# Kernel optimization log

Hardware: AMD Instinct MI355X
Metric: run time of the kernel (lower is better)

The kernel has to match this reference:

```python
import jax, jax.numpy as jnp
import numpy as np

N_EMBD = 2048
N_HEAD = 32
N_KV_HEAD = 8
HEAD_DIM = N_EMBD // N_HEAD  # 64
N_REP = N_HEAD // N_KV_HEAD  # 4
B, T = 2, 2048


def setup_inputs() -> dict:
    key = jax.random.key(0)
    ks = jax.random.split(key, 9)
    s = 1.0 / np.sqrt(N_EMBD)
    kv_dim = N_KV_HEAD * HEAD_DIM
    return {
        "x": jax.random.normal(ks[0], (B, T, N_EMBD), dtype=jnp.float32),
        "Wq": jax.random.normal(ks[1], (N_EMBD, N_EMBD), dtype=jnp.float32) * s,
        "bq": jax.random.normal(ks[2], (N_EMBD,), dtype=jnp.float32) * 0.01,
        "Wk": jax.random.normal(ks[3], (N_EMBD, kv_dim), dtype=jnp.float32) * s,
        "bk": jax.random.normal(ks[4], (kv_dim,), dtype=jnp.float32) * 0.01,
        "Wv": jax.random.normal(ks[5], (N_EMBD, kv_dim), dtype=jnp.float32) * s,
        "bv": jax.random.normal(ks[6], (kv_dim,), dtype=jnp.float32) * 0.01,
        "Wo": jax.random.normal(ks[7], (N_EMBD, N_EMBD), dtype=jnp.float32) * s,
        "bo": jax.random.normal(ks[8], (N_EMBD,), dtype=jnp.float32) * 0.01,
    }


def reference(x, Wq, bq, Wk, bk, Wv, bv, Wo, bo):
    Bsz, Tlen, C = x.shape
    # projections
    q = (x @ Wq + bq).reshape(Bsz, Tlen, N_HEAD, HEAD_DIM).transpose(0, 2, 1, 3)   # [B,H,T,d]
    k = (x @ Wk + bk).reshape(Bsz, Tlen, N_KV_HEAD, HEAD_DIM).transpose(0, 2, 1, 3)  # [B,Hkv,T,d]
    v = (x @ Wv + bv).reshape(Bsz, Tlen, N_KV_HEAD, HEAD_DIM).transpose(0, 2, 1, 3)
    # repeat_interleave KV heads to match query heads
    k = jnp.repeat(k, N_REP, axis=1)  # [B,H,T,d]
    v = jnp.repeat(v, N_REP, axis=1)
    # causal SDPA
    scale = 1.0 / jnp.sqrt(jnp.asarray(HEAD_DIM, dtype=x.dtype))
    scores = jnp.einsum('bhqd,bhkd->bhqk', q, k) * scale  # [B,H,T,T]
    causal = jnp.tril(jnp.ones((Tlen, Tlen), dtype=bool))
    scores = jnp.where(causal, scores, jnp.asarray(-jnp.inf, dtype=scores.dtype))
    attn = jax.nn.softmax(scores, axis=-1)
    y = jnp.einsum('bhqk,bhkd->bhqd', attn, v)  # [B,H,T,d]
    y = y.transpose(0, 2, 1, 3).reshape(Bsz, Tlen, C)
    return y @ Wo + bo
```

## Files before the change

kernel.cpp:

```cpp
#include <hip/hip_runtime.h>
#include <hip/hip_bf16.h>

#define B_SZ   2
#define T_SEQ  2048
#define C_EMB  2048
#define KV_DIM 512

typedef __bf16 bf16x8 __attribute__((ext_vector_type(8)));
typedef __bf16 bf16x4 __attribute__((ext_vector_type(4)));
typedef float  f32x4  __attribute__((ext_vector_type(4)));
typedef float  f32x16 __attribute__((ext_vector_type(16)));
typedef unsigned int u32;

typedef __attribute__((address_space(1))) const unsigned int gu32;
typedef __attribute__((address_space(3))) unsigned int lu32;
__device__ __forceinline__ void gload16(const void* g, void* l) {
  __builtin_amdgcn_global_load_lds((gu32*)g, (lu32*)l, 16, 0, 0);
}

__global__ __launch_bounds__(256) void cast_f32_bf16(const float* __restrict__ in,
                                                     __bf16* __restrict__ out, int n8) {
  int i = blockIdx.x * 256 + threadIdx.x;
  if (i < n8) {
    const float4* p = (const float4*)(in + (size_t)i * 8);
    float4 a = p[0], b = p[1];
    bf16x8 o;
    o[0] = (__bf16)a.x; o[1] = (__bf16)a.y; o[2] = (__bf16)a.z; o[3] = (__bf16)a.w;
    o[4] = (__bf16)b.x; o[5] = (__bf16)b.y; o[6] = (__bf16)b.z; o[7] = (__bf16)b.w;
    *(bf16x8*)(out + (size_t)i * 8) = o;
  }
}

__global__ __launch_bounds__(256) void transpose_cast_kernel(const float* __restrict__ in,
                                                             __bf16* __restrict__ out,
                                                             int R, int C) {
  __shared__ float tile[64][65];
  int c0 = blockIdx.x * 64, r0 = blockIdx.y * 64;
  int tid = threadIdx.x;
#pragma unroll
  for (int i = 0; i < 4; i++) {
    int idx = tid + i * 256;
    int row = idx >> 4;
    int c4  = (idx & 15) * 4;
    float4 v = *(const float4*)&in[(size_t)(r0 + row) * C + c0 + c4];
    tile[row][c4 + 0] = v.x; tile[row][c4 + 1] = v.y;
    tile[row][c4 + 2] = v.z; tile[row][c4 + 3] = v.w;
  }
  __syncthreads();
#pragma unroll
  for (int i = 0; i < 4; i++) {
    int idx = tid + i * 256;
    int col = idx >> 4;
    int r4  = (idx & 15) * 4;
    bf16x4 o;
    o[0] = (__bf16)tile[r4 + 0][col];
    o[1] = (__bf16)tile[r4 + 1][col];
    o[2] = (__bf16)tile[r4 + 2][col];
    o[3] = (__bf16)tile[r4 + 3][col];
    *(bf16x4*)&out[(size_t)(c0 + col) * R + r0 + r4] = o;
  }
}

__global__ __launch_bounds__(256) void concat_bias(const float* __restrict__ bq,
                                                   const float* __restrict__ bk,
                                                   const float* __restrict__ bv,
                                                   float* __restrict__ bcat) {
  int i = blockIdx.x * 256 + threadIdx.x;
  if (i < 3072) {
    float v = (i < 2048) ? bq[i] : (i < 2560 ? bk[i - 2048] : bv[i - 2560]);
    bcat[i] = v;
  }
}

template <int MODE>
__global__ __launch_bounds__(256) void gemm_bt(const __bf16* __restrict__ A,
                                               const __bf16* __restrict__ Bt,
                                               const float* __restrict__ bias,
                                               void* __restrict__ out0,
                                               __bf16* __restrict__ outK,
                                               __bf16* __restrict__ outV,
                                               int M, int N, int K) {
  __shared__ __bf16 As[128 * 32];
  __shared__ __bf16 Bs[128 * 32];
  int tid  = threadIdx.x;
  int lane = tid & 63, wave = tid >> 6;
  int wr = wave >> 1, wc = wave & 1;
  int la = lane & 15, kg = lane >> 4;
  int m0 = blockIdx.x * 128, n0 = blockIdx.y * 128;

  f32x4 acc[4][4];
#pragma unroll
  for (int i = 0; i < 4; i++)
#pragma unroll
    for (int j = 0; j < 4; j++)
#pragma unroll
      for (int r = 0; r < 4; r++) acc[i][j][r] = 0.f;

  int s0 = tid, s1 = tid + 256;
  const __bf16* ga0 = A  + (size_t)(m0 + (s0 >> 2)) * K + (s0 & 3) * 8;
  const __bf16* ga1 = A  + (size_t)(m0 + (s1 >> 2)) * K + (s1 & 3) * 8;
  const __bf16* gb0 = Bt + (size_t)(n0 + (s0 >> 2)) * K + (s0 & 3) * 8;
  const __bf16* gb1 = Bt + (size_t)(n0 + (s1 >> 2)) * K + (s1 & 3) * 8;
  __bf16* lA0 = As + (size_t)(0 * 256 + wave * 64) * 8;
  __bf16* lA1 = As + (size_t)(1 * 256 + wave * 64) * 8;
  __bf16* lB0 = Bs + (size_t)(0 * 256 + wave * 64) * 8;
  __bf16* lB1 = Bs + (size_t)(1 * 256 + wave * 64) * 8;

  for (int k0 = 0; k0 < K; k0 += 32) {
    gload16(ga0 + k0, lA0);
    gload16(ga1 + k0, lA1);
    gload16(gb0 + k0, lB0);
    gload16(gb1 + k0, lB1);
    __syncthreads();
    bf16x8 af[4], bfr[4];
#pragma unroll
    for (int i = 0; i < 4; i++) af[i]  = *(const bf16x8*)&As[(size_t)(wr * 64 + i * 16 + la) * 32 + kg * 8];
#pragma unroll
    for (int j = 0; j < 4; j++) bfr[j] = *(const bf16x8*)&Bs[(size_t)(wc * 64 + j * 16 + la) * 32 + kg * 8];
#pragma unroll
    for (int i = 0; i < 4; i++)
#pragma unroll
      for (int j = 0; j < 4; j++)
        acc[i][j] = __builtin_amdgcn_mfma_f32_16x16x32_bf16(af[i], bfr[j], acc[i][j], 0, 0, 0);
    __syncthreads();
  }

  int kgsw = ((kg & 1) << 1) | (kg >> 1);
#pragma unroll
  for (int i = 0; i < 4; i++) {
    int rowb  = m0 + wr * 64 + i * 16 + kg * 4;
    int rowbV = m0 + wr * 64 + i * 16 + kgsw * 4;
#pragma unroll
    for (int j = 0; j < 4; j++) {
      int col = n0 + wc * 64 + j * 16 + la;
      float bv = bias[col];
#pragma unroll
      for (int r = 0; r < 4; r++) {
        float v = acc[i][j][r] + bv;
        if (MODE == 2) {
          ((float*)out0)[(size_t)(rowb + r) * N + col] = v;
        } else {
          if (n0 < 2048)      ((__bf16*)out0)[(size_t)(rowb + r) * 2048 + col] = (__bf16)(v * 0.18033688f);
          else if (n0 < 2560) outK[(size_t)(rowb + r) * 512 + (col - 2048)] = (__bf16)v;
          else                outV[(size_t)(col - 2560) * M + rowbV + r] = (__bf16)v;
        }
      }
    }
  }
}

__global__ __launch_bounds__(128) void attn_kernel(const __bf16* __restrict__ Q,
                                                   const __bf16* __restrict__ K,
                                                   const __bf16* __restrict__ Vt,
                                                   __bf16* __restrict__ Y) {
  __shared__ __bf16 Ylds[2][32][72];
  const int M = B_SZ * T_SEQ;
  int tid = threadIdx.x;
  int wv = tid >> 6, l = tid & 63;
  int qcol = l & 31, hh = l >> 5;
  int g = blockIdx.x;
  int swz = (g & 7) * 128 + (g >> 3);
  int bh = swz >> 4, pi2 = swz & 15;
  int pi = pi2 * 2 + wv;
  int b = bh >> 5, hq = bh & 31, kvh = hq >> 2;

  const __bf16* kbase = K + (size_t)(b * T_SEQ + qcol) * KV_DIM + kvh * 64 + hh * 8;
  const __bf16* vb0 = Vt + (size_t)(kvh * 64 + qcol) * M + (size_t)b * T_SEQ + hh * 8;
  const __bf16* vb1 = vb0 + (size_t)32 * M;
  __bf16 (*slab)[72] = Ylds[wv];

  for (int halfi = 0; halfi < 2; ++halfi) {
    int qt = halfi ? (63 - pi) : pi;
    int q0 = qt * 32;

    const __bf16* qrow = Q + (size_t)(b * T_SEQ + q0 + qcol) * C_EMB + hq * 64;
    bf16x8 qf[4];
#pragma unroll
    for (int c = 0; c < 4; c++) qf[c] = *(const bf16x8*)(qrow + c * 16 + hh * 8);

    f32x16 acc0, acc1;
#pragma unroll
    for (int r = 0; r < 16; r++) { acc0[r] = 0.f; acc1[r] = 0.f; }
    float m_run = -1e30f, l_run = 0.f;

    bf16x8 kf[4];
#pragma unroll
    for (int c = 0; c < 4; c++) kf[c] = *(const bf16x8*)(kbase + c * 16);

    for (int kb = 0; kb <= q0; kb += 32) {
      f32x16 s;
#pragma unroll
      for (int r = 0; r < 16; r++) s[r] = 0.f;
      __builtin_amdgcn_s_setprio(1);
#pragma unroll
      for (int c = 0; c < 4; c++)
        s = __builtin_amdgcn_mfma_f32_32x32x16_bf16(kf[c], qf[c], s, 0, 0, 0);
      __builtin_amdgcn_s_setprio(0);
      {
        int nkb = (kb + 32 <= q0) ? kb + 32 : 0;
        const __bf16* nk = kbase + (size_t)nkb * KV_DIM;
#pragma unroll
        for (int c = 0; c < 4; c++) kf[c] = *(const bf16x8*)(nk + c * 16);
      }
      bf16x8 vf0 = *(const bf16x8*)(vb0 + kb);
      bf16x8 vf1 = *(const bf16x8*)(vb0 + kb + 16);
      bf16x8 vf2 = *(const bf16x8*)(vb1 + kb);
      bf16x8 vf3 = *(const bf16x8*)(vb1 + kb + 16);
      if (kb == q0) {
#pragma unroll
        for (int r = 0; r < 16; r++) {
          int kr = (r & 3) + 8 * (r >> 2) + 4 * hh;
          s[r] = (kr <= qcol) ? s[r] : -1e30f;
        }
      }
      float m01 = fmaxf(s[0], s[1]),  m23 = fmaxf(s[2], s[3]);
      float m45 = fmaxf(s[4], s[5]),  m67 = fmaxf(s[6], s[7]);
      float m89 = fmaxf(s[8], s[9]),  mab = fmaxf(s[10], s[11]);
      float mcd = fmaxf(s[12], s[13]), mef = fmaxf(s[14], s[15]);
      float mloc = fmaxf(fmaxf(fmaxf(m01, m23), fmaxf(m45, m67)),
                         fmaxf(fmaxf(m89, mab), fmaxf(mcd, mef)));
      mloc = fmaxf(mloc, __shfl_xor(mloc, 32, 64));
      if (__any(mloc > m_run + 6.0f)) {
        float mnew = fmaxf(m_run, mloc);
        float corr = exp2f(m_run - mnew);
        l_run *= corr;
#pragma unroll
        for (int r = 0; r < 16; r++) { acc0[r] *= corr; acc1[r] *= corr; }
        m_run = mnew;
      }
#pragma unroll
      for (int r = 0; r < 16; r++) s[r] = exp2f(s[r] - m_run);
      l_run += (((s[0] + s[1]) + (s[2] + s[3])) + ((s[4] + s[5]) + (s[6] + s[7])))
             + (((s[8] + s[9]) + (s[10] + s[11])) + ((s[12] + s[13]) + (s[14] + s[15])));
      union { u32 u[4]; bf16x8 v; } w0u, w1u;
#pragma unroll
      for (int j = 0; j < 4; j++) {
        union { __bf16 b2[2]; u32 u; } p0, p1;
        p0.b2[0] = (__bf16)s[2 * j];     p0.b2[1] = (__bf16)s[2 * j + 1];
        p1.b2[0] = (__bf16)s[8 + 2 * j]; p1.b2[1] = (__bf16)s[9 + 2 * j];
        w0u.u[j] = p0.u;
        w1u.u[j] = p1.u;
      }
      __builtin_amdgcn_s_setprio(1);
      acc0 = __builtin_amdgcn_mfma_f32_32x32x16_bf16(vf0, w0u.v, acc0, 0, 0, 0);
      acc0 = __builtin_amdgcn_mfma_f32_32x32x16_bf16(vf1, w1u.v, acc0, 0, 0, 0);
      acc1 = __builtin_amdgcn_mfma_f32_32x32x16_bf16(vf2, w0u.v, acc1, 0, 0, 0);
      acc1 = __builtin_amdgcn_mfma_f32_32x32x16_bf16(vf3, w1u.v, acc1, 0, 0, 0);
      __builtin_amdgcn_s_setprio(0);
    }

    l_run += __shfl_xor(l_run, 32, 64);
    float inv = 1.0f / l_run;
#pragma unroll
    for (int r = 0; r < 16; r++) {
      int drow = (r & 3) + 8 * (r >> 2) + 4 * hh;
      slab[qcol][drow]      = (__bf16)(acc0[r] * inv);
      slab[qcol][32 + drow] = (__bf16)(acc1[r] * inv);
    }
    __bf16* yrow = Y + (size_t)(b * T_SEQ + q0 + qcol) * C_EMB + hq * 64 + hh * 32;
#pragma unroll
    for (int c = 0; c < 4; c++)
      *(bf16x8*)(yrow + c * 8) = *(const bf16x8*)&slab[qcol][hh * 32 + c * 8];
  }
}

extern "C" void kernel_launch(void* const* d_in, const int* in_sizes, int n_in,
                              void* d_out, int out_size, void* d_ws, size_t ws_size,
                              hipStream_t stream) {
  const float* x  = (const float*)d_in[0];
  const float* Wq = (const float*)d_in[1];
  const float* bq = (const float*)d_in[2];
  const float* Wk = (const float*)d_in[3];
  const float* bk = (const float*)d_in[4];
  const float* Wv = (const float*)d_in[5];
  const float* bv = (const float*)d_in[6];
  const float* Wo = (const float*)d_in[7];
  const float* bo = (const float*)d_in[8];
  float* out = (float*)d_out;

  const int M = B_SZ * T_SEQ;

  char* w = (char*)d_ws;
  __bf16* xb   = (__bf16*)w; w += (size_t)M * C_EMB * 2;
  __bf16* Wall = (__bf16*)w; w += (size_t)3072 * C_EMB * 2;
  __bf16* Wot  = (__bf16*)w; w += (size_t)C_EMB * C_EMB * 2;
  float*  bcat = (float*)w;  w += (size_t)3072 * 4;
  __bf16* qb   = (__bf16*)w; w += (size_t)M * C_EMB * 2;
  __bf16* kbf  = (__bf16*)w; w += (size_t)M * KV_DIM * 2;
  __bf16* vbt  = (__bf16*)w; w += (size_t)KV_DIM * M * 2;
  __bf16* yb   = (__bf16*)w; w += (size_t)M * C_EMB * 2;

  cast_f32_bf16<<<(M * C_EMB / 8 + 255) / 256, 256, 0, stream>>>(x, xb, M * C_EMB / 8);

  transpose_cast_kernel<<<dim3(C_EMB / 64, C_EMB / 64), 256, 0, stream>>>(Wq, Wall, C_EMB, C_EMB);
  transpose_cast_kernel<<<dim3(KV_DIM / 64, C_EMB / 64), 256, 0, stream>>>(Wk, Wall + (size_t)2048 * C_EMB, C_EMB, KV_DIM);
  transpose_cast_kernel<<<dim3(KV_DIM / 64, C_EMB / 64), 256, 0, stream>>>(Wv, Wall + (size_t)2560 * C_EMB, C_EMB, KV_DIM);
  transpose_cast_kernel<<<dim3(C_EMB / 64, C_EMB / 64), 256, 0, stream>>>(Wo, Wot, C_EMB, C_EMB);
  concat_bias<<<12, 256, 0, stream>>>(bq, bk, bv, bcat);

  gemm_bt<1><<<dim3(M / 128, 3072 / 128), 256, 0, stream>>>(xb, Wall, bcat, qb, kbf, vbt, M, 3072, C_EMB);

  attn_kernel<<<dim3(1024), 128, 0, stream>>>(qb, kbf, vbt, yb);

  gemm_bt<2><<<dim3(M / 128, C_EMB / 128), 256, 0, stream>>>(yb, Wot, bo, out, nullptr, nullptr, M, C_EMB, C_EMB);
}
```

Baseline: 377.8 us.

## Split attention KV range across two waves with LDS softmax merge

```diff
diff --git a/kernel.cpp b/kernel.cpp
--- a/kernel.cpp
+++ b/kernel.cpp
@@ -149,118 +149,139 @@
   }
 }
 
-__global__ __launch_bounds__(128) void attn_kernel(const __bf16* __restrict__ Q,
-                                                   const __bf16* __restrict__ K,
-                                                   const __bf16* __restrict__ Vt,
-                                                   __bf16* __restrict__ Y) {
-  __shared__ __bf16 Ylds[2][32][72];
+__global__ __launch_bounds__(128, 5) void attn_kernel(const __bf16* __restrict__ Q,
+                                                      const __bf16* __restrict__ K,
+                                                      const __bf16* __restrict__ Vt,
+                                                      __bf16* __restrict__ Y) {
+  __shared__ float accX[2][16][64];
+  __shared__ float mLm[2][32], mLl[2][32];
+  __shared__ __bf16 slab[32][72];
   const int M = B_SZ * T_SEQ;
   int tid = threadIdx.x;
   int wv = tid >> 6, l = tid & 63;
   int qcol = l & 31, hh = l >> 5;
   int g = blockIdx.x;
-  int swz = (g & 7) * 128 + (g >> 3);
-  int bh = swz >> 4, pi2 = swz & 15;
-  int pi = pi2 * 2 + wv;
+  int swz = (g & 7) * 512 + (g >> 3);
+  int bh = swz >> 6;
+  int qt = 63 - (swz & 63);
   int b = bh >> 5, hq = bh & 31, kvh = hq >> 2;
+  int q0 = qt * 32;
+  int nt = qt + 1;
+  int tA = wv ? (nt >> 1) : 0;
+  int tB = wv ? nt : (nt >> 1);
+  int kb0 = tA * 32, kb1 = tB * 32;
+
+  const __bf16* qrow = Q + (size_t)(b * T_SEQ + q0 + qcol) * C_EMB + hq * 64;
+  bf16x8 qf[4];
+#pragma unroll
+  for (int c = 0; c < 4; c++) qf[c] = *(const bf16x8*)(qrow + c * 16 + hh * 8);
+
+  f32x16 acc0, acc1;
+#pragma unroll
+  for (int r = 0; r < 16; r++) { acc0[r] = 0.f; acc1[r] = 0.f; }
+  float m_run = -1e30f, l_run = 0.f;
 
   const __bf16* kbase = K + (size_t)(b * T_SEQ + qcol) * KV_DIM + kvh * 64 + hh * 8;
   const __bf16* vb0 = Vt + (size_t)(kvh * 64 + qcol) * M + (size_t)b * T_SEQ + hh * 8;
   const __bf16* vb1 = vb0 + (size_t)32 * M;
-  __bf16 (*slab)[72] = Ylds[wv];
-
-  for (int halfi = 0; halfi < 2; ++halfi) {
-    int qt = halfi ? (63 - pi) : pi;
-    int q0 = qt * 32;
-
-    const __bf16* qrow = Q + (size_t)(b * T_SEQ + q0 + qcol) * C_EMB + hq * 64;
-    bf16x8 qf[4];
-#pragma unroll
-    for (int c = 0; c < 4; c++) qf[c] = *(const bf16x8*)(qrow + c * 16 + hh * 8);
-
-    f32x16 acc0, acc1;
-#pragma unroll
-    for (int r = 0; r < 16; r++) { acc0[r] = 0.f; acc1[r] = 0.f; }
-    float m_run = -1e30f, l_run = 0.f;
-
-    bf16x8 kf[4];
-#pragma unroll
-    for (int c = 0; c < 4; c++) kf[c] = *(const bf16x8*)(kbase + c * 16);
-
-    for (int kb = 0; kb <= q0; kb += 32) {
-      f32x16 s;
-#pragma unroll
-      for (int r = 0; r < 16; r++) s[r] = 0.f;
-      __builtin_amdgcn_s_setprio(1);
-#pragma unroll
-      for (int c = 0; c < 4; c++)
-        s = __builtin_amdgcn_mfma_f32_32x32x16_bf16(kf[c], qf[c], s, 0, 0, 0);
-      __builtin_amdgcn_s_setprio(0);
-      {
-        int nkb = (kb + 32 <= q0) ? kb + 32 : 0;
-        const __bf16* nk = kbase + (size_t)nkb * KV_DIM;
-#pragma unroll
-        for (int c = 0; c < 4; c++) kf[c] = *(const bf16x8*)(nk + c * 16);
+
+  bf16x8 kf[4];
+  {
+    int kbs = (kb0 < kb1) ? kb0 : 0;
+    const __bf16* kp = kbase + (size_t)kbs * KV_DIM;
+#pragma unroll
+    for (int c = 0; c < 4; c++) kf[c] = *(const bf16x8*)(kp + c * 16);
+  }
+
+  for (int kb = kb0; kb < kb1; kb += 32) {
+    f32x16 s;
+#pragma unroll
+    for (int r = 0; r < 16; r++) s[r] = 0.f;
+    __builtin_amdgcn_s_setprio(1);
+#pragma unroll
+    for (int c = 0; c < 4; c++)
+      s = __builtin_amdgcn_mfma_f32_32x32x16_bf16(kf[c], qf[c], s, 0, 0, 0);
+    __builtin_amdgcn_s_setprio(0);
+    {
+      int nkb = (kb + 32 < kb1) ? kb + 32 : kb0;
+      const __bf16* nk = kbase + (size_t)nkb * KV_DIM;
+#pragma unroll
+      for (int c = 0; c < 4; c++) kf[c] = *(const bf16x8*)(nk + c * 16);
+    }
+    bf16x8 vf0 = *(const bf16x8*)(vb0 + kb);
+    bf16x8 vf1 = *(const bf16x8*)(vb0 + kb + 16);
+    bf16x8 vf2 = *(const bf16x8*)(vb1 + kb);
+    bf16x8 vf3 = *(const bf16x8*)(vb1 + kb + 16);
+    if (kb == q0) {
+#pragma unroll
+      for (int r = 0; r < 16; r++) {
+        int kr = (r & 3) + 8 * (r >> 2) + 4 * hh;
+        s[r] = (kr <= qcol) ? s[r] : -1e30f;
       }
-      bf16x8 vf0 = *(const bf16x8*)(vb0 + kb);
-      bf16x8 vf1 = *(const bf16x8*)(vb0 + kb + 16);
-      bf16x8 vf2 = *(const bf16x8*)(vb1 + kb);
-      bf16x8 vf3 = *(const bf16x8*)(vb1 + kb + 16);
-      if (kb == q0) {
-#pragma unroll
-        for (int r = 0; r < 16; r++) {
-          int kr = (r & 3) + 8 * (r >> 2) + 4 * hh;
-          s[r] = (kr <= qcol) ? s[r] : -1e30f;
-        }
-      }
-      float m01 = fmaxf(s[0], s[1]),  m23 = fmaxf(s[2], s[3]);
-      float m45 = fmaxf(s[4], s[5]),  m67 = fmaxf(s[6], s[7]);
-      float m89 = fmaxf(s[8], s[9]),  mab = fmaxf(s[10], s[11]);
-      float mcd = fmaxf(s[12], s[13]), mef = fmaxf(s[14], s[15]);
-      float mloc = fmaxf(fmaxf(fmaxf(m01, m23), fmaxf(m45, m67)),
-                         fmaxf(fmaxf(m89, mab), fmaxf(mcd, mef)));
-      mloc = fmaxf(mloc, __shfl_xor(mloc, 32, 64));
-      if (__any(mloc > m_run + 6.0f)) {
-        float mnew = fmaxf(m_run, mloc);
-        float corr = exp2f(m_run - mnew);
-        l_run *= corr;
-#pragma unroll
-        for (int r = 0; r < 16; r++) { acc0[r] *= corr; acc1[r] *= corr; }
-        m_run = mnew;
-      }
-#pragma unroll
-      for (int r = 0; r < 16; r++) s[r] = exp2f(s[r] - m_run);
-      l_run += (((s[0] + s[1]) + (s[2] + s[3])) + ((s[4] + s[5]) + (s[6] + s[7])))
-             + (((s[8] + s[9]) + (s[10] + s[11])) + ((s[12] + s[13]) + (s[14] + s[15])));
-      union { u32 u[4]; bf16x8 v; } w0u, w1u;
-#pragma unroll
-      for (int j = 0; j < 4; j++) {
-        union { __bf16 b2[2]; u32 u; } p0, p1;
-        p0.b2[0] = (__bf16)s[2 * j];     p0.b2[1] = (__bf16)s[2 * j + 1];
-        p1.b2[0] = (__bf16)s[8 + 2 * j]; p1.b2[1] = (__bf16)s[9 + 2 * j];
-        w0u.u[j] = p0.u;
-        w1u.u[j] = p1.u;
-      }
-      __builtin_amdgcn_s_setprio(1);
-      acc0 = __builtin_amdgcn_mfma_f32_32x32x16_bf16(vf0, w0u.v, acc0, 0, 0, 0);
-      acc0 = __builtin_amdgcn_mfma_f32_32x32x16_bf16(vf1, w1u.v, acc0, 0, 0, 0);
-      acc1 = __builtin_amdgcn_mfma_f32_32x32x16_bf16(vf2, w0u.v, acc1, 0, 0, 0);
-      acc1 = __builtin_amdgcn_mfma_f32_32x32x16_bf16(vf3, w1u.v, acc1, 0, 0, 0);
-      __builtin_amdgcn_s_setprio(0);
-    }
-
-    l_run += __shfl_xor(l_run, 32, 64);
-    float inv = 1.0f / l_run;
+    }
+    float m01 = fmaxf(s[0], s[1]),  m23 = fmaxf(s[2], s[3]);
+    float m45 = fmaxf(s[4], s[5]),  m67 = fmaxf(s[6], s[7]);
+    float m89 = fmaxf(s[8], s[9]),  mab = fmaxf(s[10], s[11]);
+    float mcd = fmaxf(s[12], s[13]), mef = fmaxf(s[14], s[15]);
+    float mloc = fmaxf(fmaxf(fmaxf(m01, m23), fmaxf(m45, m67)),
+                       fmaxf(fmaxf(m89, mab), fmaxf(mcd, mef)));
+    mloc = fmaxf(mloc, __shfl_xor(mloc, 32, 64));
+    if (__any(mloc > m_run + 6.0f)) {
+      float mnew = fmaxf(m_run, mloc);
+      float corr = exp2f(m_run - mnew);
+      l_run *= corr;
+#pragma unroll
+      for (int r = 0; r < 16; r++) { acc0[r] *= corr; acc1[r] *= corr; }
+      m_run = mnew;
+    }
+#pragma unroll
+    for (int r = 0; r < 16; r++) s[r] = exp2f(s[r] - m_run);
+    l_run += (((s[0] + s[1]) + (s[2] + s[3])) + ((s[4] + s[5]) + (s[6] + s[7])))
+           + (((s[8] + s[9]) + (s[10] + s[11])) + ((s[12] + s[13]) + (s[14] + s[15])));
+    union { u32 u[4]; bf16x8 v; } w0u, w1u;
+#pragma unroll
+    for (int j = 0; j < 4; j++) {
+      union { __bf16 b2[2]; u32 u; } p0, p1;
+      p0.b2[0] = (__bf16)s[2 * j];     p0.b2[1] = (__bf16)s[2 * j + 1];
+      p1.b2[0] = (__bf16)s[8 + 2 * j]; p1.b2[1] = (__bf16)s[9 + 2 * j];
+      w0u.u[j] = p0.u;
+      w1u.u[j] = p1.u;
+    }
+    __builtin_amdgcn_s_setprio(1);
+    acc0 = __builtin_amdgcn_mfma_f32_32x32x16_bf16(vf0, w0u.v, acc0, 0, 0, 0);
+    acc0 = __builtin_amdgcn_mfma_f32_32x32x16_bf16(vf1, w1u.v, acc0, 0, 0, 0);
+    acc1 = __builtin_amdgcn_mfma_f32_32x32x16_bf16(vf2, w0u.v, acc1, 0, 0, 0);
+    acc1 = __builtin_amdgcn_mfma_f32_32x32x16_bf16(vf3, w1u.v, acc1, 0, 0, 0);
+    __builtin_amdgcn_s_setprio(0);
+  }
+
+  l_run += __shfl_xor(l_run, 32, 64);
+  {
+    f32x16 accO = wv ? acc0 : acc1;
+#pragma unroll
+    for (int r = 0; r < 16; r++) accX[wv][r][l] = accO[r];
+    if (hh == 0) { mLm[wv][qcol] = m_run; mLl[wv][qcol] = l_run; }
+  }
+  __syncthreads();
+  {
+    float mo = mLm[wv ^ 1][qcol], lo = mLl[wv ^ 1][qcol];
+    float mm = fmaxf(m_run, mo);
+    float cs = exp2f(m_run - mm), co = exp2f(mo - mm);
+    float inv = 1.0f / (cs * l_run + co * lo);
+    f32x16 mine = wv ? acc1 : acc0;
 #pragma unroll
     for (int r = 0; r < 16; r++) {
-      int drow = (r & 3) + 8 * (r >> 2) + 4 * hh;
-      slab[qcol][drow]      = (__bf16)(acc0[r] * inv);
-      slab[qcol][32 + drow] = (__bf16)(acc1[r] * inv);
-    }
-    __bf16* yrow = Y + (size_t)(b * T_SEQ + q0 + qcol) * C_EMB + hq * 64 + hh * 32;
-#pragma unroll
-    for (int c = 0; c < 4; c++)
-      *(bf16x8*)(yrow + c * 8) = *(const bf16x8*)&slab[qcol][hh * 32 + c * 8];
+      float v = (cs * mine[r] + co * accX[wv ^ 1][r][l]) * inv;
+      int drow = (r & 3) + 8 * (r >> 2) + 4 * hh + 32 * wv;
+      slab[qcol][drow] = (__bf16)v;
+    }
+  }
+  __syncthreads();
+  {
+    int qc = tid >> 2, seg = tid & 3;
+    __bf16* yrow = Y + (size_t)(b * T_SEQ + q0 + qc) * C_EMB + hq * 64 + seg * 8;
+    *(bf16x8*)(yrow)      = *(const bf16x8*)&slab[qc][seg * 8];
+    *(bf16x8*)(yrow + 32) = *(const bf16x8*)&slab[qc][seg * 8 + 32];
   }
 }
 
@@ -300,7 +321,7 @@
 
   gemm_bt<1><<<dim3(M / 128, 3072 / 128), 256, 0, stream>>>(xb, Wall, bcat, qb, kbf, vbt, M, 3072, C_EMB);
 
-  attn_kernel<<<dim3(1024), 128, 0, stream>>>(qb, kbf, vbt, yb);
+  attn_kernel<<<dim3(4096), 128, 0, stream>>>(qb, kbf, vbt, yb);
 
   gemm_bt<2><<<dim3(M / 128, C_EMB / 128), 256, 0, stream>>>(yb, Wot, bo, out, nullptr, nullptr, M, C_EMB, C_EMB);
 }
```

New measurement: 540.7 us. 1.43x slower.
